# Performance work log

Hardware: AMD Instinct MI355X
Metric: run time of the kernel (lower is better)

The kernel has to match this reference:

```python
import jax, jax.numpy as jnp
import numpy as np

SCALE = 56  # output spatial resolution, HW = 3136
K = 3       # n_neighbors for top-k softmin scoring


def avg_pool3(x):
    # F.avg_pool2d(x, 3, 1, 1) with count_include_pad=True -> zero-padded sum / 9
    s = jax.lax.reduce_window(x, 0.0, jax.lax.add, (1, 1, 3, 3), (1, 1, 1, 1),
                              ((0, 0), (0, 0), (1, 1), (1, 1)))
    return s / 9.0


def resize_to(x, hw):
    # F.interpolate(mode='bilinear', align_corners=False) == jax.image half-pixel bilinear
    B, C, _, _ = x.shape
    return jax.image.resize(x, (B, C, hw, hw), method='bilinear')


def add_coords(x):
    # CoordConv AddCoords: append normalized x/y coordinate channels in [-1, 1]
    B, C, H, W = x.shape
    xx = jnp.broadcast_to(jnp.linspace(-1.0, 1.0, W, dtype=x.dtype)[None, :], (H, W))
    yy = jnp.broadcast_to(jnp.linspace(-1.0, 1.0, H, dtype=x.dtype)[:, None], (H, W))
    xxb = jnp.broadcast_to(xx[None, None], (B, 1, H, W))
    yyb = jnp.broadcast_to(yy[None, None], (B, 1, H, W))
    return jnp.concatenate([x, xxb, yyb], axis=1)


def setup_inputs() -> dict:
    key = jax.random.key(0)
    k1, k2, k3, k4, k5 = jax.random.split(key, 5)
    p1 = jax.random.normal(k1, (8, 256, 56, 56), dtype=jnp.float32)
    p2 = jax.random.normal(k2, (8, 512, 28, 28), dtype=jnp.float32)
    p3 = jax.random.normal(k3, (8, 1024, 14, 14), dtype=jnp.float32)
    W = jax.random.normal(k4, (1792, 1794), dtype=jnp.float32) * 0.02  # 1x1 CoordConv weight
    b = jnp.zeros((1792,), dtype=jnp.float32)
    C = jax.random.normal(k5, (1792, 3136), dtype=jnp.float32) * 0.05  # centroid bank
    return {"p1": p1, "p2": p2, "p3": p3, "W": W, "b": b, "C": C}


def reference(p1, p2, p3, W, b, C):
    # Descriptor: smooth each pyramid level, upsample to 56x56, concat -> (B,1792,56,56)
    o1 = avg_pool3(p1)
    o2 = resize_to(avg_pool3(p2), SCALE)
    o3 = resize_to(avg_pool3(p3), SCALE)
    sample = jnp.concatenate([o1, o2, o3], axis=1)
    # CoordConv 1x1
    xc = add_coords(sample)  # (B, 1794, 56, 56)
    phi = jnp.einsum('bchw,oc->bohw', xc, W) + b[None, :, None, None]
    B = phi.shape[0]
    phi_p = phi.reshape(B, 1792, SCALE * SCALE).transpose(0, 2, 1)  # (B, HW, C)
    # pairwise squared distances via expansion + matmul: (B, HW, 3136)
    features = jnp.sum(phi_p * phi_p, axis=2, keepdims=True)
    centers = jnp.sum(C * C, axis=0, keepdims=True)
    dist = features + centers - 2.0 * jnp.matmul(phi_p, C)
    dist = jnp.sqrt(jnp.maximum(dist, 0.0))
    # top-K smallest distances (ascending, like torch.topk(largest=False))
    vals = -jax.lax.top_k(-dist, K)[0]  # (B, HW, K)
    w = jax.nn.softmax(-vals, axis=-1)  # softmin
    score = w[..., 0] * vals[..., 0]    # (B, HW)
    score = score.reshape(B, 1, SCALE, SCALE)
    return score
```

## Files before the change

kernel.cpp:

```cpp
#include <hip/hip_runtime.h>
#include <math.h>
#include <stdint.h>

typedef float f32x4 __attribute__((ext_vector_type(4)));
typedef short short8 __attribute__((ext_vector_type(8)));

static constexpr int HWo   = 3136;
static constexpr int NB    = 8;
static constexpr int NP    = 3200;
static constexpr int KDIM  = 1794;
static constexpr int KP1   = 1856;
static constexpr int ODIM  = 1792;
static constexpr int NCENT = 3136;
static constexpr int NHB   = 50;
static constexpr int NHBV  = 49;

__device__ __forceinline__ uint16_t f2bf(float f) {
  union { float f; uint32_t u; } v; v.f = f;
  uint32_t u = v.u;
  return (uint16_t)((u + 0x7FFFu + ((u >> 16) & 1u)) >> 16);
}
__device__ __forceinline__ float bf2f(uint16_t h) {
  union { uint32_t u; float f; } v; v.u = ((uint32_t)h) << 16;
  return v.f;
}

__device__ __forceinline__ void gld16(const uint16_t* __restrict__ g, uint16_t* l) {
  __builtin_amdgcn_global_load_lds(
      (const __attribute__((address_space(1))) uint16_t*)g,
      (__attribute__((address_space(3))) uint16_t*)l,
      16, 0, 0);
}

__device__ __forceinline__ int xcd_swizzle(int bid, int nwg) {
  int q = nwg >> 3, r = nwg & 7;
  int xcd = bid & 7, idx = bid >> 3;
  int base = (xcd < r) ? xcd * (q + 1) : r * (q + 1) + (xcd - r) * q;
  return base + idx;
}

__global__ __launch_bounds__(256) void convW_kernel(const float* __restrict__ W, uint16_t* __restrict__ Wh) {
  int idx = blockIdx.x * 256 + threadIdx.x;
  int o = idx / KP1, k = idx % KP1;
  float v = (k < KDIM) ? W[(size_t)o * KDIM + k] : 0.f;
  Wh[idx] = f2bf(v);
}

__global__ __launch_bounds__(256) void convC_kernel(const float* __restrict__ C, uint16_t* __restrict__ Ct) {
  __shared__ float tile[64][65];
  int bj = blockIdx.x * 64;
  int bo = blockIdx.y * 64;
  int tx = threadIdx.x & 63, ty = threadIdx.x >> 6;
  #pragma unroll
  for (int s = 0; s < 16; ++s) {
    int o = ty + s * 4;
    tile[o][tx] = C[(size_t)(bo + o) * NCENT + bj + tx];
  }
  __syncthreads();
  #pragma unroll
  for (int s = 0; s < 16; ++s) {
    int j = ty + s * 4;
    Ct[(size_t)(bj + j) * ODIM + bo + tx] = f2bf(tile[tx][j]);
  }
}

__global__ __launch_bounds__(256) void rownorm_kernel(const uint16_t* __restrict__ src, float* __restrict__ dst) {
  int t = threadIdx.x, lane = t & 63, wave = t >> 6;
  int row = blockIdx.x * 4 + wave;
  const uint32_t* p = (const uint32_t*)(src + (size_t)row * ODIM);
  float s = 0.f;
  #pragma unroll
  for (int it = 0; it < 14; ++it) {
    uint32_t u = p[it * 64 + lane];
    float a = bf2f((uint16_t)(u & 0xFFFF)), b = bf2f((uint16_t)(u >> 16));
    s += a * a + b * b;
  }
  #pragma unroll
  for (int m = 1; m < 64; m <<= 1) s += __shfl_xor(s, m, 64);
  if (lane == 0) dst[row] = s;
}

__global__ __launch_bounds__(256) void zerof_kernel(float* __restrict__ p, int n) {
  int i = blockIdx.x * 256 + threadIdx.x;
  if (i < n) p[i] = 0.f;
}

static constexpr int P1SZ = 256 * 3136;
static constexpr int P2SZ = 512 * 784;
static constexpr int P3SZ = 1024 * 196;
static constexpr int PT23 = P2SZ + P3SZ;

__device__ __forceinline__ float pool9f(const float* __restrict__ p, int S, int y, int x) {
  float s = 0.f;
  for (int dy = -1; dy <= 1; ++dy) {
    int yy = y + dy; if (yy < 0 || yy >= S) continue;
    for (int dx = -1; dx <= 1; ++dx) {
      int xx = x + dx; if (xx < 0 || xx >= S) continue;
      s += p[yy * S + xx];
    }
  }
  return s * (1.f / 9.f);
}

__global__ __launch_bounds__(256) void pool_kernel(const float* __restrict__ p2, const float* __restrict__ p3,
                                                   float* __restrict__ pooled, int g0) {
  int b = g0 + blockIdx.y;
  float* pb = pooled + (size_t)blockIdx.y * PT23;
  int idx = blockIdx.x * 256 + threadIdx.x;
  const float* src; int S, loc;
  if (idx < P2SZ) { src = p2 + (size_t)b * P2SZ; S = 28; loc = idx; }
  else            { src = p3 + (size_t)b * P3SZ; S = 14; loc = idx - P2SZ; }
  int c = loc / (S * S), hw = loc % (S * S);
  pb[idx] = pool9f(src + (size_t)c * S * S, S, hw / S, hw % S);
}

__global__ __launch_bounds__(256) void asmA_kernel(const float* __restrict__ p1, uint16_t* __restrict__ xcb, int g0) {
  __shared__ float tile[64][65];
  int bg = blockIdx.z;
  const float* src = p1 + (size_t)(g0 + bg) * P1SZ;
  uint16_t* xb = xcb + (size_t)bg * NP * KP1;
  int p0 = blockIdx.x * 64;
  int c0 = blockIdx.y * 64;
  int tx = threadIdx.x & 63, ty = threadIdx.x >> 6;
  #pragma unroll
  for (int s = 0; s < 16; ++s) {
    int c = ty + s * 4;
    int p = p0 + tx;
    tile[c][tx] = pool9f(src + (size_t)(c0 + c) * HWo, 56, p / 56, p % 56);
  }
  __syncthreads();
  #pragma unroll
  for (int s = 0; s < 16; ++s) {
    int p = ty + s * 4;
    xb[(size_t)(p0 + p) * KP1 + c0 + tx] = f2bf(tile[tx][p]);
  }
}

__global__ __launch_bounds__(256) void asmB_kernel(const float* __restrict__ pooled, uint16_t* __restrict__ xcb) {
  __shared__ float rows[2][128][29];
  int bg = blockIdx.z;
  const float* pb = pooled + (size_t)bg * PT23;
  uint16_t* xb = xcb + (size_t)bg * NP * KP1;
  int y = blockIdx.x;
  int ct = blockIdx.y;
  bool lvl2 = ct < 4;
  int S = lvl2 ? 28 : 14;
  float scale = lvl2 ? 0.5f : 0.25f;
  float shift = lvl2 ? -0.25f : -0.375f;
  int chbase = lvl2 ? 256 + ct * 128 : 768 + (ct - 4) * 128;
  const float* base = lvl2 ? pb + (size_t)(ct * 128) * 784
                           : pb + P2SZ + (size_t)((ct - 4) * 128) * 196;
  int planesz = S * S;
  float sy = y * scale + shift;
  float fy0 = floorf(sy);
  float fy = sy - fy0;
  int y0 = (int)fy0, y1 = y0 + 1;
  y0 = y0 < 0 ? 0 : y0; y1 = y1 > S - 1 ? S - 1 : y1;
  int t = threadIdx.x;
  int tot = 128 * 2 * S;
  for (int idx = t; idx < tot; idx += 256) {
    int r = idx / S, e = idx - r * S;
    int c = r >> 1, yr = r & 1;
    rows[yr][c][e] = base[(size_t)c * planesz + (yr ? y1 : y0) * S + e];
  }
  __syncthreads();
  int c = t & 127, xs = t >> 7;
  #pragma unroll
  for (int xi = 0; xi < 28; ++xi) {
    int x = xi * 2 + xs;
    float sx = x * scale + shift;
    float fx0 = floorf(sx);
    float fx = sx - fx0;
    int x0 = (int)fx0, x1 = x0 + 1;
    x0 = x0 < 0 ? 0 : x0; x1 = x1 > S - 1 ? S - 1 : x1;
    float v00 = rows[0][c][x0], v01 = rows[0][c][x1];
    float v10 = rows[1][c][x0], v11 = rows[1][c][x1];
    float v = (1.f - fy) * ((1.f - fx) * v00 + fx * v01) + fy * ((1.f - fx) * v10 + fx * v11);
    xb[(size_t)(y * 56 + x) * KP1 + chbase + c] = f2bf(v);
  }
}

__global__ __launch_bounds__(256) void asmC_kernel(uint16_t* __restrict__ xcb) {
  int bg = blockIdx.y;
  uint16_t* xb = xcb + (size_t)bg * NP * KP1;
  int idx = blockIdx.x * 256 + threadIdx.x;
  int i = idx >> 6, ch = 1792 + (idx & 63);
  int x = i % 56, y = i / 56;
  float v = (ch == 1792) ? (-1.f + 2.f * x / 55.f)
          : (ch == 1793) ? (-1.f + 2.f * y / 55.f) : 0.f;
  xb[(size_t)i * KP1 + ch] = f2bf(v);
}

__global__ __launch_bounds__(256) void gemm1_mfma(const uint16_t* __restrict__ Wh, const float* __restrict__ bias,
                                                  const uint16_t* __restrict__ xcb, uint16_t* __restrict__ phi_t,
                                                  float* __restrict__ feat) {
  __shared__ union { uint16_t ab[2][128][64]; uint16_t tr[128][136]; } sm;
  int wid = xcd_swizzle(blockIdx.x, gridDim.x);
  int row0 = (wid % 14) * 128;
  int col0 = (wid / 14) * 128;
  int t = threadIdx.x;
  int lane = t & 63, wave = t >> 6;
  int wm = wave & 1, wn = wave >> 1;
  int l15 = lane & 15, quad = lane >> 4;
  int rr = wave * 8 + (lane >> 3);
  int sg = ((lane & 7) ^ (lane >> 3)) * 8;
  f32x4 acc[4][4] = {};
  for (int k0 = 0; k0 < KP1; k0 += 64) {
    #pragma unroll
    for (int i = 0; i < 4; ++i) {
      gld16(&Wh [(size_t)(row0 + i * 32 + rr) * KP1 + k0 + sg], &sm.ab[0][i * 32 + wave * 8][0]);
      gld16(&xcb[(size_t)(col0 + i * 32 + rr) * KP1 + k0 + sg], &sm.ab[1][i * 32 + wave * 8][0]);
    }
    __syncthreads();
    #pragma unroll
    for (int kk = 0; kk < 2; ++kk) {
      short8 a[4], b[4];
      #pragma unroll
      for (int i = 0; i < 4; ++i) {
        int r = wm * 64 + i * 16 + l15;
        a[i] = *(const short8*)&sm.ab[0][r][((quad + 4 * kk) ^ (r & 7)) * 8];
      }
      #pragma unroll
      for (int j = 0; j < 4; ++j) {
        int r = wn * 64 + j * 16 + l15;
        b[j] = *(const short8*)&sm.ab[1][r][((quad + 4 * kk) ^ (r & 7)) * 8];
      }
      #pragma unroll
      for (int i = 0; i < 4; ++i)
        #pragma unroll
        for (int j = 0; j < 4; ++j)
          acc[i][j] = __builtin_amdgcn_mfma_f32_16x16x32_bf16(a[i], b[j], acc[i][j], 0, 0, 0);
    }
    __syncthreads();
  }
  #pragma unroll
  for (int i = 0; i < 4; ++i) {
    int o4 = wm * 64 + i * 16 + quad * 4;
    float4 bv = *(const float4*)&bias[row0 + o4];
    #pragma unroll
    for (int j = 0; j < 4; ++j) {
      int p = wn * 64 + j * 16 + l15;
      ushort4 u;
      u.x = f2bf(acc[i][j][0] + bv.x);
      u.y = f2bf(acc[i][j][1] + bv.y);
      u.z = f2bf(acc[i][j][2] + bv.z);
      u.w = f2bf(acc[i][j][3] + bv.w);
      *(ushort4*)&sm.tr[p][o4] = u;
    }
  }
  __syncthreads();
  int c = t & 15, prb = t >> 4;
  #pragma unroll
  for (int s = 0; s < 8; ++s) {
    int pr = s * 16 + prb;
    uint4 v = *(const uint4*)&sm.tr[pr][c * 8];
    *(uint4*)&phi_t[(size_t)(col0 + pr) * ODIM + row0 + c * 8] = v;
    const uint16_t* pv = (const uint16_t*)&v;
    float ssq = 0.f;
    #pragma unroll
    for (int e = 0; e < 8; ++e) { float f = bf2f(pv[e]); ssq += f * f; }
    #pragma unroll
    for (int m = 1; m < 16; m <<= 1) ssq += __shfl_xor(ssq, m, 16);
    if (c == 0) atomicAdd(&feat[col0 + pr], ssq);
  }
}

__device__ __forceinline__ void ins3(float v, float& a, float& b, float& c) {
  if (v < c) {
    if (v < b) { c = b; if (v < a) { b = a; a = v; } else { b = v; } }
    else { c = v; }
  }
}

__global__ __launch_bounds__(256) void gemm2_mfma(const uint16_t* __restrict__ phi_t, const uint16_t* __restrict__ Ct,
                                                  const float* __restrict__ cent, float* __restrict__ partial) {
  __shared__ uint16_t As[128][64];
  __shared__ uint16_t Bs[128][64];
  int wid = xcd_swizzle(blockIdx.x, gridDim.x);
  int band = wid / 125, l = wid % 125;
  int stc = l / 25, sp = l % 25;
  int row0 = (band * 5 + sp / 5) * 128;
  int col0 = (stc * 5 + sp % 5) * 128;
  int t = threadIdx.x;
  int lane = t & 63, wave = t >> 6;
  int wc = wave & 1;
  int wp = wave >> 1;
  int l15 = lane & 15, quad = lane >> 4;
  int rr = wave * 8 + (lane >> 3);
  int sg = ((lane & 7) ^ (lane >> 3)) * 8;
  f32x4 acc[4][4] = {};
  for (int k0 = 0; k0 < ODIM; k0 += 64) {
    #pragma unroll
    for (int i = 0; i < 4; ++i) {
      gld16(&phi_t[(size_t)(row0 + i * 32 + rr) * ODIM + k0 + sg], &As[i * 32 + wave * 8][0]);
      gld16(&Ct   [(size_t)(col0 + i * 32 + rr) * ODIM + k0 + sg], &Bs[i * 32 + wave * 8][0]);
    }
    __syncthreads();
    #pragma unroll
    for (int kk = 0; kk < 2; ++kk) {
      short8 ac[4], bp[4];
      #pragma unroll
      for (int i = 0; i < 4; ++i) {
        int r = wc * 64 + i * 16 + l15;
        ac[i] = *(const short8*)&Bs[r][((quad + 4 * kk) ^ (r & 7)) * 8];
      }
      #pragma unroll
      for (int j = 0; j < 4; ++j) {
        int r = wp * 64 + j * 16 + l15;
        bp[j] = *(const short8*)&As[r][((quad + 4 * kk) ^ (r & 7)) * 8];
      }
      #pragma unroll
      for (int i = 0; i < 4; ++i)
        #pragma unroll
        for (int j = 0; j < 4; ++j)
          acc[i][j] = __builtin_amdgcn_mfma_f32_16x16x32_bf16(ac[i], bp[j], acc[i][j], 0, 0, 0);
    }
    __syncthreads();
  }
  if (col0 + wc * 64 < NCENT) {
    float4 cv[4];
    #pragma unroll
    for (int i = 0; i < 4; ++i)
      cv[i] = *(const float4*)&cent[col0 + wc * 64 + i * 16 + quad * 4];
    int hb = (col0 >> 6) + wc;
    #pragma unroll
    for (int j = 0; j < 4; ++j) {
      float t0 = 3.4e38f, t1 = 3.4e38f, t2 = 3.4e38f;
      #pragma unroll
      for (int i = 0; i < 4; ++i) {
        float c4[4] = {cv[i].x, cv[i].y, cv[i].z, cv[i].w};
        #pragma unroll
        for (int r = 0; r < 4; ++r)
          ins3(c4[r] - 2.f * acc[i][j][r], t0, t1, t2);
      }
      #pragma unroll
      for (int m = 16; m < 64; m <<= 1) {
        float u0 = __shfl_xor(t0, m, 64);
        float u1 = __shfl_xor(t1, m, 64);
        float u2 = __shfl_xor(t2, m, 64);
        ins3(u0, t0, t1, t2); ins3(u1, t0, t1, t2); ins3(u2, t0, t1, t2);
      }
      if (quad == 0) {
        int pix = row0 + wp * 64 + j * 16 + l15;
        float* pp = &partial[((size_t)pix * NHB + hb) * 3];
        pp[0] = t0; pp[1] = t1; pp[2] = t2;
      }
    }
  }
}

__global__ __launch_bounds__(256) void score_kernel(const float* __restrict__ partial, const float* __restrict__ feat,
                                                    float* __restrict__ out, int g0) {
  int t = threadIdx.x, lane = t & 63, wave = t >> 6;
  int gi = blockIdx.x * 4 + wave;
  int bg = gi / HWo, row = gi - bg * HWo;
  int grow = bg * NP + row;
  float t0 = 3.4e38f, t1 = 3.4e38f, t2 = 3.4e38f;
  if (lane < NHBV) {
    const float* pp = &partial[((size_t)grow * NHB + lane) * 3];
    ins3(pp[0], t0, t1, t2); ins3(pp[1], t0, t1, t2); ins3(pp[2], t0, t1, t2);
  }
  #pragma unroll
  for (int m = 1; m < 64; m <<= 1) {
    float u0 = __shfl_xor(t0, m, 64);
    float u1 = __shfl_xor(t1, m, 64);
    float u2 = __shfl_xor(t2, m, 64);
    ins3(u0, t0, t1, t2); ins3(u1, t0, t1, t2); ins3(u2, t0, t1, t2);
  }
  if (lane == 0) {
    float ft = feat[grow];
    float v0 = sqrtf(fmaxf(ft + t0, 0.f));
    float v1 = sqrtf(fmaxf(ft + t1, 0.f));
    float v2 = sqrtf(fmaxf(ft + t2, 0.f));
    float w0 = 1.f / (1.f + expf(v0 - v1) + expf(v0 - v2));
    out[(size_t)(g0 + bg) * HWo + row] = v0 * w0;
  }
}

extern "C" void kernel_launch(void* const* d_in, const int* in_sizes, int n_in,
                              void* d_out, int out_size, void* d_ws, size_t ws_size,
                              hipStream_t stream) {
  const float* p1   = (const float*)d_in[0];
  const float* p2   = (const float*)d_in[1];
  const float* p3   = (const float*)d_in[2];
  const float* Wm   = (const float*)d_in[3];
  const float* bias = (const float*)d_in[4];
  const float* Cm   = (const float*)d_in[5];
  float* out = (float*)d_out;

  const size_t szWh   = (size_t)ODIM * KP1 * 2;
  const size_t szCt   = (size_t)NP * ODIM * 2;
  const size_t szCent = (size_t)NP * 4;
  const size_t szXcb  = (size_t)NP * KP1 * 2;
  const size_t szPhi  = (size_t)NP * ODIM * 2;
  const size_t szPart = (size_t)NP * NHB * 3 * 4;
  const size_t szFeat = (size_t)NP * 4;
  const size_t fixedSz = szWh + szCt + szCent;
  const size_t perSz   = szXcb + szPhi + szPart + szFeat;
  int GB = 8;
  while (GB > 1 && fixedSz + perSz * (size_t)GB > ws_size) GB >>= 1;

  char* ws = (char*)d_ws;
  size_t off = 0;
  uint16_t* Wh     = (uint16_t*)(ws + off); off += szWh;
  uint16_t* Ct     = (uint16_t*)(ws + off); off += szCt;
  float*    cent   = (float*)(ws + off);    off += szCent;
  uint16_t* xcb    = (uint16_t*)(ws + off); off += szXcb * GB;
  uint16_t* phi_t  = (uint16_t*)(ws + off);
  float*    pooled = (float*)(ws + off);    off += szPhi * GB;
  float*    partial= (float*)(ws + off);    off += szPart * GB;
  float*    feat   = (float*)(ws + off);    off += szFeat * GB;

  convW_kernel<<<(ODIM * KP1) / 256, 256, 0, stream>>>(Wm, Wh);
  convC_kernel<<<dim3(NCENT / 64, ODIM / 64), 256, 0, stream>>>(Cm, Ct);
  rownorm_kernel<<<784, 256, 0, stream>>>(Ct, cent);

  for (int g0 = 0; g0 < NB; g0 += GB) {
    pool_kernel<<<dim3(PT23 / 256, GB), 256, 0, stream>>>(p2, p3, pooled, g0);
    asmA_kernel<<<dim3(HWo / 64, 4, GB), 256, 0, stream>>>(p1, xcb, g0);
    asmB_kernel<<<dim3(56, 12, GB), 256, 0, stream>>>(pooled, xcb);
    asmC_kernel<<<dim3((HWo * 64) / 256, GB), 256, 0, stream>>>(xcb);
    zerof_kernel<<<(NP * GB) / 256, 256, 0, stream>>>(feat, NP * GB);
    gemm1_mfma<<<GB * 25 * 14, 256, 0, stream>>>(Wh, bias, xcb, phi_t, feat);
    gemm2_mfma<<<GB * 25 * 25, 256, 0, stream>>>(phi_t, Ct, cent, partial);
    score_kernel<<<GB * HWo / 4, 256, 0, stream>>>(partial, feat, out, g0);
  }
}
```

Before: 1.000 ms.

## Fuse zeroing and coord channels into pool kernels; row-tile asmA pooling via LDS

Removes the separate zerof and asmC kernel launches by folding feat zeroing into pool_kernel and coord-channel writes into asmB. asmA is restructured to process one output row per block, loading three input rows into shared memory so the 3x3 pooling reuses neighbours instead of issuing nine global loads per output. This cuts launch overhead and redundant global reads. It adds a dependency: pool_kernel's grid must cover NP*GB, which holds since PT23 is much larger.

```diff
diff --git a/kernel.cpp b/kernel.cpp
--- a/kernel.cpp
+++ b/kernel.cpp
@@ -80,11 +80,6 @@
   if (lane == 0) dst[row] = s;
 }
 
-__global__ __launch_bounds__(256) void zerof_kernel(float* __restrict__ p, int n) {
-  int i = blockIdx.x * 256 + threadIdx.x;
-  if (i < n) p[i] = 0.f;
-}
-
 static constexpr int P1SZ = 256 * 3136;
 static constexpr int P2SZ = 512 * 784;
 static constexpr int P3SZ = 1024 * 196;
@@ -103,10 +98,12 @@
 }
 
 __global__ __launch_bounds__(256) void pool_kernel(const float* __restrict__ p2, const float* __restrict__ p3,
-                                                   float* __restrict__ pooled, int g0) {
+                                                   float* __restrict__ pooled, float* __restrict__ feat,
+                                                   int nfeat, int g0) {
   int b = g0 + blockIdx.y;
   float* pb = pooled + (size_t)blockIdx.y * PT23;
   int idx = blockIdx.x * 256 + threadIdx.x;
+  if (blockIdx.y == 0 && idx < nfeat) feat[idx] = 0.f;
   const float* src; int S, loc;
   if (idx < P2SZ) { src = p2 + (size_t)b * P2SZ; S = 28; loc = idx; }
   else            { src = p3 + (size_t)b * P3SZ; S = 14; loc = idx - P2SZ; }
@@ -115,24 +112,33 @@
 }
 
 __global__ __launch_bounds__(256) void asmA_kernel(const float* __restrict__ p1, uint16_t* __restrict__ xcb, int g0) {
-  __shared__ float tile[64][65];
+  __shared__ float rows[3][64][57];
   int bg = blockIdx.z;
   const float* src = p1 + (size_t)(g0 + bg) * P1SZ;
   uint16_t* xb = xcb + (size_t)bg * NP * KP1;
-  int p0 = blockIdx.x * 64;
+  int y = blockIdx.x;
   int c0 = blockIdx.y * 64;
-  int tx = threadIdx.x & 63, ty = threadIdx.x >> 6;
-  #pragma unroll
-  for (int s = 0; s < 16; ++s) {
-    int c = ty + s * 4;
-    int p = p0 + tx;
-    tile[c][tx] = pool9f(src + (size_t)(c0 + c) * HWo, 56, p / 56, p % 56);
+  int t = threadIdx.x;
+  for (int i = 0; i < 42; ++i) {
+    int idx = i * 256 + t;
+    int r = idx / 3584, rem = idx - r * 3584;
+    int c = rem / 56, e = rem - c * 56;
+    int ys = y - 1 + r;
+    rows[r][c][e] = (ys >= 0 && ys < 56) ? src[(size_t)(c0 + c) * HWo + ys * 56 + e] : 0.f;
   }
   __syncthreads();
   #pragma unroll
-  for (int s = 0; s < 16; ++s) {
-    int p = ty + s * 4;
-    xb[(size_t)(p0 + p) * KP1 + c0 + tx] = f2bf(tile[tx][p]);
+  for (int i = 0; i < 14; ++i) {
+    int idx = i * 256 + t;
+    int c = idx & 63, x = idx >> 6;
+    float s = 0.f;
+    #pragma unroll
+    for (int r = 0; r < 3; ++r) {
+      s += rows[r][c][x];
+      if (x > 0)  s += rows[r][c][x - 1];
+      if (x < 55) s += rows[r][c][x + 1];
+    }
+    xb[(size_t)(y * 56 + x) * KP1 + c0 + c] = f2bf(s * (1.f / 9.f));
   }
 }
 
@@ -178,17 +184,16 @@
     float v = (1.f - fy) * ((1.f - fx) * v00 + fx * v01) + fy * ((1.f - fx) * v10 + fx * v11);
     xb[(size_t)(y * 56 + x) * KP1 + chbase + c] = f2bf(v);
   }
-}
-
-__global__ __launch_bounds__(256) void asmC_kernel(uint16_t* __restrict__ xcb) {
-  int bg = blockIdx.y;
-  uint16_t* xb = xcb + (size_t)bg * NP * KP1;
-  int idx = blockIdx.x * 256 + threadIdx.x;
-  int i = idx >> 6, ch = 1792 + (idx & 63);
-  int x = i % 56, y = i / 56;
-  float v = (ch == 1792) ? (-1.f + 2.f * x / 55.f)
-          : (ch == 1793) ? (-1.f + 2.f * y / 55.f) : 0.f;
-  xb[(size_t)i * KP1 + ch] = f2bf(v);
+  if (ct == 0) {
+    #pragma unroll
+    for (int i = 0; i < 14; ++i) {
+      int idx = i * 256 + t;
+      int cho = idx & 63, x = idx >> 6;
+      float v = (cho == 0) ? (-1.f + 2.f * x / 55.f)
+              : (cho == 1) ? (-1.f + 2.f * y / 55.f) : 0.f;
+      xb[(size_t)(y * 56 + x) * KP1 + 1792 + cho] = f2bf(v);
+    }
+  }
 }
 
 __global__ __launch_bounds__(256) void gemm1_mfma(const uint16_t* __restrict__ Wh, const float* __restrict__ bias,
@@ -416,11 +421,9 @@
   rownorm_kernel<<<784, 256, 0, stream>>>(Ct, cent);
 
   for (int g0 = 0; g0 < NB; g0 += GB) {
-    pool_kernel<<<dim3(PT23 / 256, GB), 256, 0, stream>>>(p2, p3, pooled, g0);
-    asmA_kernel<<<dim3(HWo / 64, 4, GB), 256, 0, stream>>>(p1, xcb, g0);
+    pool_kernel<<<dim3(PT23 / 256, GB), 256, 0, stream>>>(p2, p3, pooled, feat, NP * GB, g0);
+    asmA_kernel<<<dim3(56, 4, GB), 256, 0, stream>>>(p1, xcb, g0);
     asmB_kernel<<<dim3(56, 12, GB), 256, 0, stream>>>(pooled, xcb);
-    asmC_kernel<<<dim3((HWo * 64) / 256, GB), 256, 0, stream>>>(xcb);
-    zerof_kernel<<<(NP * GB) / 256, 256, 0, stream>>>(feat, NP * GB);
     gemm1_mfma<<<GB * 25 * 14, 256, 0, stream>>>(Wh, bias, xcb, phi_t, feat);
     gemm2_mfma<<<GB * 25 * 25, 256, 0, stream>>>(phi_t, Ct, cent, partial);
     score_kernel<<<GB * HWo / 4, 256, 0, stream>>>(partial, feat, out, g0);
```

New measurement: 1.006 ms. About the same (+0.5%).
